# Kernel optimization log

Measured on AMD Instinct MI355X. Metric: run time of the kernel, lower is better.

Reference implementation:

```python
import jax, jax.numpy as jnp
import numpy as np

INF = 1e10  # sentinel 'infinity' for non-feature pixels (safe to add (s*N)^2 without overflow)


def _edt_sq_last(f, s):
    """Exact 1D squared distance transform along the last axis.
    f: (..., N) initialized to 0 at feature pixels, INF elsewhere.
    Returns g[..., i] = min_j f[..., j] + (s*(i-j))^2.
    Sequential lax.scan over output positions keeps memory at O(N) extra."""
    N = f.shape[-1]
    j = jnp.arange(N, dtype=f.dtype)

    def step(_, i):
        return None, jnp.min(f + (s * (i - j)) ** 2, axis=-1)

    _, out = jax.lax.scan(step, None, jnp.arange(N, dtype=f.dtype))
    return jnp.moveaxis(out, 0, -1)


def _edt(feature_mask, sampling):
    """Euclidean distance to the nearest True pixel of feature_mask (2D, anisotropic sampling).
    Equivalent to scipy.ndimage.distance_transform_edt(~feature_mask, sampling=sampling)."""
    f = jnp.where(feature_mask, 0.0, INF).astype(jnp.float32)
    # pass over axis -2 (rows), then axis -1 (cols) -- exact separable squared EDT
    f = jnp.moveaxis(_edt_sq_last(jnp.moveaxis(f, -2, -1), sampling[0]), -1, -2)
    f = _edt_sq_last(f, sampling[1])
    return jnp.sqrt(f)


def _distance_map(y_onehot, sampling):
    """res = edt_to_pos * negmask - (edt_to_neg - 1) * posmask, 0 where class absent."""
    pos = y_onehot              # (B,K,H,W) bool
    neg = ~pos
    d_neg = _edt(pos, sampling)  # distance of neg pixels to nearest pos pixel
    d_pos = _edt(neg, sampling)  # distance of pos pixels to nearest neg pixel
    res = jnp.where(neg, d_neg, 0.0) - jnp.where(pos, d_pos - 1.0, 0.0)
    has_pos = pos.any(axis=(-2, -1), keepdims=True)  # scipy path leaves res[k]=0 if class absent
    return jnp.where(has_pos, res, 0.0)


def reference(x, y):
    # x: (B,K,H,W) float; y: (B,1,H,W) int labels in [0,K)
    K = x.shape[1]
    y_onehot = (y == jnp.arange(K, dtype=y.dtype)[None, :, None, None])  # scatter_ onehot
    dist_map = jax.lax.stop_gradient(_distance_map(y_onehot, (1.0, 1.0)))
    return jnp.mean(x * dist_map)  # einsum('bkwh,bkwh->bkwh').mean()


def setup_inputs() -> dict:
    key = jax.random.key(0)
    k1, k2 = jax.random.split(key)
    x = jax.random.normal(k1, (8, 4, 256, 256), dtype=jnp.float32)
    y = jax.random.randint(k2, (8, 1, 256, 256), 0, 4, dtype=jnp.int32)
    return {"x": x, "y": y}
```

## Files before the change

### kernel.cpp

```cpp
#include <hip/hip_runtime.h>


#define HH 256
#define WW 256
#define NPIX (HH*WW)
#define NPM 64
#define BIG (1 << 27)

#define SEGS 16
#define RSEG 16
#define CPB 16

__global__ __launch_bounds__(256, 4) void edt_vpass(
        const int* __restrict__ y, unsigned short* __restrict__ g) {
    __shared__ unsigned short d[HH][CPB + 1];
    __shared__ short segLast[SEGS][CPB];
    __shared__ short segFirst[SEGS][CPB];

    int bid   = blockIdx.x;
    int pm    = bid >> 4;
    int cc    = bid & 15;
    int which = pm & 1;
    int plane = pm >> 1;
    int b     = plane >> 2;
    int k     = plane & 3;

    int t   = threadIdx.x;
    int col = t & (CPB - 1);
    int seg = t >> 4;
    int w   = cc * CPB + col;
    int h0  = seg * RSEG;

    const int* yp = y + b * NPIX;
    unsigned short* gp = g + (size_t)pm * NPIX;

    int lastL = -1000, firstL = 1000;
    for (int i = 0; i < RSEG; ++i) {
        int h   = h0 + i;
        int lab = yp[h * WW + w];
        int feat = ((lab == k) ? 1 : 0) ^ which;
        if (feat) { lastL = h; if (firstL > 900) firstL = h; }
        d[h][col] = (unsigned short)min(h - lastL, 1000);
    }
    segLast[seg][col]  = (short)lastL;
    segFirst[seg][col] = (short)firstL;
    __syncthreads();

    int prevLast = -1000;
    for (int s = seg - 1; s >= 0; --s) {
        int v = segLast[s][col];
        if (v >= 0) { prevLast = v; break; }
    }
    int nextFirst = 1000;
    for (int s = seg + 1; s < SEGS; ++s) {
        int v = segFirst[s][col];
        if (v < 900) { nextFirst = v; break; }
    }

    int nd = nextFirst;
    for (int i = RSEG - 1; i >= 0; --i) {
        int h  = h0 + i;
        int du = d[h][col];
        if (du == 0) nd = h;
        int dup = min(du, h - prevLast);
        int ddn = nd - h;
        int m   = min(min(dup, ddn), 256);
        gp[h * WW + w] = (m > 255) ? (unsigned short)0xFFFF
                                   : (unsigned short)(m * m);
    }
}

#define ROWS_PER_BLK 8
#define NBLK2 2048

__global__ void edt_hpass(const unsigned short* __restrict__ g,
                          const float* __restrict__ x,
                          double* __restrict__ bsums) {
    __shared__ int tile[ROWS_PER_BLK][WW];
    __shared__ double wsum[4];

    int bid   = blockIdx.x;
    int pm    = bid >> 5;
    int rc    = bid & 31;
    int r0    = rc * ROWS_PER_BLK;
    int which = pm & 1;
    int plane = pm >> 1;
    int t     = threadIdx.x;

    const unsigned short* gp = g + (size_t)pm * NPIX;
    const float* xp = x + (size_t)plane * NPIX;

    const unsigned int* gp32 = (const unsigned int*)(gp + r0 * WW);
    #pragma unroll
    for (int i2 = 0; i2 < 4; ++i2) {
        int idx = i2 * 256 + t;
        int row = idx >> 7;
        int c2  = idx & 127;
        unsigned int v = gp32[row * 128 + c2];
        int v0 = (int)(v & 0xFFFFu);
        int v1 = (int)(v >> 16);
        tile[row][2 * c2]     = (v0 == 0xFFFF) ? BIG : v0;
        tile[row][2 * c2 + 1] = (v1 == 0xFFFF) ? BIG : v1;
    }
    __syncthreads();

    double lsum = 0.0;
    for (int i = 0; i < ROWS_PER_BLK; ++i) {
        int best = tile[i][t];
        #pragma unroll 1
        for (int bs = 1; bs < WW; bs += 4) {
            if (bs * bs >= best) break;
            int m = best;
            #pragma unroll
            for (int u = 0; u < 4; ++u) {
                int r  = bs + u;
                int rr = r * r;
                int jl = max(t - r, 0);
                int jr = min(t + r, WW - 1);
                m = min(m, tile[i][jl] + rr);
                m = min(m, tile[i][jr] + rr);
            }
            best = m;
        }
        if (best > 0 && best < BIG) {
            float xv   = xp[(r0 + i) * WW + t];
            float dd   = sqrtf((float)best);
            float term = which ? (1.0f - dd) : dd;
            lsum += (double)(xv * term);
        }
    }

    for (int off = 32; off > 0; off >>= 1)
        lsum += __shfl_down(lsum, off, 64);
    int lane = t & 63, wv = t >> 6;
    if (lane == 0) wsum[wv] = lsum;
    __syncthreads();
    if (t == 0) bsums[bid] = wsum[0] + wsum[1] + wsum[2] + wsum[3];
}

__global__ void edt_finalize(const double* __restrict__ bsums, float* __restrict__ out) {
    __shared__ double wsum[4];
    int t = threadIdx.x;
    double s = 0.0;
    for (int i = t; i < NBLK2; i += 256) s += bsums[i];
    for (int off = 32; off > 0; off >>= 1)
        s += __shfl_down(s, off, 64);
    int lane = t & 63, wv = t >> 6;
    if (lane == 0) wsum[wv] = s;
    __syncthreads();
    if (t == 0)
        out[0] = (float)((wsum[0] + wsum[1] + wsum[2] + wsum[3]) * (1.0 / 2097152.0));
}

extern "C" void kernel_launch(void* const* d_in, const int* in_sizes, int n_in,
                              void* d_out, int out_size, void* d_ws, size_t ws_size,
                              hipStream_t stream) {
    const float* x = (const float*)d_in[0];
    const int*   y = (const int*)d_in[1];
    float* out = (float*)d_out;

    unsigned short* g = (unsigned short*)d_ws;
    double* bsums = (double*)((char*)d_ws + (size_t)NPM * NPIX * sizeof(unsigned short));

    edt_vpass   <<<1024,  256, 0, stream>>>(y, g);
    edt_hpass   <<<NBLK2, 256, 0, stream>>>(g, x, bsums);
    edt_finalize<<<1,     256, 0, stream>>>(bsums, out);
}
```

Baseline: 74.49 us.

## Process positive and negative masks together in one block per plane

Both the vertical and horizontal EDT passes now handle the feature mask and its complement in the same thread, packing the two 16-bit squared distances into one 32-bit word. This halves the number of blocks, reads the labels and x only once per plane, and merges the two contributions per pixel before accumulating. The cost is that each block does twice the serial work, with more registers and shared memory and fewer blocks to spread across the GPU. In the horizontal pass the two search loops run one after the other, so their trip counts add up per thread.

```diff
diff --git a/kernel.cpp b/kernel.cpp
--- a/kernel.cpp
+++ b/kernel.cpp
@@ -4,7 +4,7 @@
 #define HH 256
 #define WW 256
 #define NPIX (HH*WW)
-#define NPM 64
+#define NPL 32
 #define BIG (1 << 27)
 
 #define SEGS 16
@@ -12,18 +12,16 @@
 #define CPB 16
 
 __global__ __launch_bounds__(256, 4) void edt_vpass(
-        const int* __restrict__ y, unsigned short* __restrict__ g) {
-    __shared__ unsigned short d[HH][CPB + 1];
-    __shared__ short segLast[SEGS][CPB];
-    __shared__ short segFirst[SEGS][CPB];
+        const int* __restrict__ y, unsigned int* __restrict__ g) {
+    __shared__ unsigned int d[HH][CPB + 1];
+    __shared__ short segLast0[SEGS][CPB], segFirst0[SEGS][CPB];
+    __shared__ short segLast1[SEGS][CPB], segFirst1[SEGS][CPB];
 
-    int bid   = blockIdx.x;
-    int pm    = bid >> 4;
-    int cc    = bid & 15;
-    int which = pm & 1;
-    int plane = pm >> 1;
-    int b     = plane >> 2;
-    int k     = plane & 3;
+    int bid = blockIdx.x;
+    int pm  = bid >> 4;
+    int cc  = bid & 15;
+    int b   = pm >> 2;
+    int k   = pm & 3;
 
     int t   = threadIdx.x;
     int col = t & (CPB - 1);
@@ -32,100 +30,128 @@
     int h0  = seg * RSEG;
 
     const int* yp = y + b * NPIX;
-    unsigned short* gp = g + (size_t)pm * NPIX;
+    unsigned int* gp = g + (size_t)pm * NPIX;
 
-    int lastL = -1000, firstL = 1000;
+    int last0 = -1000, first0 = 1000, last1 = -1000, first1 = 1000;
     for (int i = 0; i < RSEG; ++i) {
         int h   = h0 + i;
         int lab = yp[h * WW + w];
-        int feat = ((lab == k) ? 1 : 0) ^ which;
-        if (feat) { lastL = h; if (firstL > 900) firstL = h; }
-        d[h][col] = (unsigned short)min(h - lastL, 1000);
+        if (lab == k) { last0 = h; if (first0 > 900) first0 = h; }
+        else          { last1 = h; if (first1 > 900) first1 = h; }
+        unsigned int du0 = (unsigned int)min(h - last0, 1000);
+        unsigned int du1 = (unsigned int)min(h - last1, 1000);
+        d[h][col] = du0 | (du1 << 16);
     }
-    segLast[seg][col]  = (short)lastL;
-    segFirst[seg][col] = (short)firstL;
+    segLast0[seg][col] = (short)last0;  segFirst0[seg][col] = (short)first0;
+    segLast1[seg][col] = (short)last1;  segFirst1[seg][col] = (short)first1;
     __syncthreads();
 
-    int prevLast = -1000;
+    int prevLast0 = -1000, prevLast1 = -1000;
     for (int s = seg - 1; s >= 0; --s) {
-        int v = segLast[s][col];
-        if (v >= 0) { prevLast = v; break; }
+        int v = segLast0[s][col];
+        if (v >= 0) { prevLast0 = v; break; }
     }
-    int nextFirst = 1000;
+    for (int s = seg - 1; s >= 0; --s) {
+        int v = segLast1[s][col];
+        if (v >= 0) { prevLast1 = v; break; }
+    }
+    int nextFirst0 = 1000, nextFirst1 = 1000;
     for (int s = seg + 1; s < SEGS; ++s) {
-        int v = segFirst[s][col];
-        if (v < 900) { nextFirst = v; break; }
+        int v = segFirst0[s][col];
+        if (v < 900) { nextFirst0 = v; break; }
+    }
+    for (int s = seg + 1; s < SEGS; ++s) {
+        int v = segFirst1[s][col];
+        if (v < 900) { nextFirst1 = v; break; }
     }
 
-    int nd = nextFirst;
+    int nd0 = nextFirst0, nd1 = nextFirst1;
     for (int i = RSEG - 1; i >= 0; --i) {
-        int h  = h0 + i;
-        int du = d[h][col];
-        if (du == 0) nd = h;
-        int dup = min(du, h - prevLast);
-        int ddn = nd - h;
-        int m   = min(min(dup, ddn), 256);
-        gp[h * WW + w] = (m > 255) ? (unsigned short)0xFFFF
-                                   : (unsigned short)(m * m);
+        int h = h0 + i;
+        unsigned int pk = d[h][col];
+        int du0 = (int)(pk & 0xFFFFu), du1 = (int)(pk >> 16);
+        if (du0 == 0) nd0 = h;
+        if (du1 == 0) nd1 = h;
+        int m0 = min(min(min(du0, h - prevLast0), nd0 - h), 256);
+        int m1 = min(min(min(du1, h - prevLast1), nd1 - h), 256);
+        unsigned int v0 = (m0 > 255) ? 0xFFFFu : (unsigned int)(m0 * m0);
+        unsigned int v1 = (m1 > 255) ? 0xFFFFu : (unsigned int)(m1 * m1);
+        gp[h * WW + w] = v0 | (v1 << 16);
     }
 }
 
 #define ROWS_PER_BLK 8
-#define NBLK2 2048
+#define NBLK2 1024
 
-__global__ void edt_hpass(const unsigned short* __restrict__ g,
+__global__ void edt_hpass(const unsigned int* __restrict__ g,
                           const float* __restrict__ x,
                           double* __restrict__ bsums) {
-    __shared__ int tile[ROWS_PER_BLK][WW];
+    __shared__ int t0[ROWS_PER_BLK][WW];
+    __shared__ int t1[ROWS_PER_BLK][WW];
     __shared__ double wsum[4];
 
-    int bid   = blockIdx.x;
-    int pm    = bid >> 5;
-    int rc    = bid & 31;
-    int r0    = rc * ROWS_PER_BLK;
-    int which = pm & 1;
-    int plane = pm >> 1;
-    int t     = threadIdx.x;
+    int bid = blockIdx.x;
+    int pm  = bid >> 5;
+    int rc  = bid & 31;
+    int r0  = rc * ROWS_PER_BLK;
+    int t   = threadIdx.x;
 
-    const unsigned short* gp = g + (size_t)pm * NPIX;
-    const float* xp = x + (size_t)plane * NPIX;
+    const unsigned int* gp = g + (size_t)pm * NPIX + r0 * WW;
+    const float* xp = x + (size_t)pm * NPIX;
 
-    const unsigned int* gp32 = (const unsigned int*)(gp + r0 * WW);
     #pragma unroll
-    for (int i2 = 0; i2 < 4; ++i2) {
+    for (int i2 = 0; i2 < 8; ++i2) {
         int idx = i2 * 256 + t;
-        int row = idx >> 7;
-        int c2  = idx & 127;
-        unsigned int v = gp32[row * 128 + c2];
+        int row = idx >> 8;
+        int c   = idx & 255;
+        unsigned int v = gp[row * WW + c];
         int v0 = (int)(v & 0xFFFFu);
         int v1 = (int)(v >> 16);
-        tile[row][2 * c2]     = (v0 == 0xFFFF) ? BIG : v0;
-        tile[row][2 * c2 + 1] = (v1 == 0xFFFF) ? BIG : v1;
+        t0[row][c] = (v0 == 0xFFFF) ? BIG : v0;
+        t1[row][c] = (v1 == 0xFFFF) ? BIG : v1;
     }
     __syncthreads();
 
     double lsum = 0.0;
     for (int i = 0; i < ROWS_PER_BLK; ++i) {
-        int best = tile[i][t];
+        int best0 = t0[i][t];
         #pragma unroll 1
         for (int bs = 1; bs < WW; bs += 4) {
-            if (bs * bs >= best) break;
-            int m = best;
+            if (bs * bs >= best0) break;
+            int m = best0;
             #pragma unroll
             for (int u = 0; u < 4; ++u) {
                 int r  = bs + u;
                 int rr = r * r;
                 int jl = max(t - r, 0);
                 int jr = min(t + r, WW - 1);
-                m = min(m, tile[i][jl] + rr);
-                m = min(m, tile[i][jr] + rr);
+                m = min(m, t0[i][jl] + rr);
+                m = min(m, t0[i][jr] + rr);
             }
-            best = m;
+            best0 = m;
         }
-        if (best > 0 && best < BIG) {
+        int best1 = t1[i][t];
+        #pragma unroll 1
+        for (int bs = 1; bs < WW; bs += 4) {
+            if (bs * bs >= best1) break;
+            int m = best1;
+            #pragma unroll
+            for (int u = 0; u < 4; ++u) {
+                int r  = bs + u;
+                int rr = r * r;
+                int jl = max(t - r, 0);
+                int jr = min(t + r, WW - 1);
+                m = min(m, t1[i][jl] + rr);
+                m = min(m, t1[i][jr] + rr);
+            }
+            best1 = m;
+        }
+        bool c0 = (best0 > 0) && (best0 < BIG);
+        bool c1 = (best1 > 0) && (best1 < BIG);
+        if (c0 | c1) {
             float xv   = xp[(r0 + i) * WW + t];
-            float dd   = sqrtf((float)best);
-            float term = which ? (1.0f - dd) : dd;
+            float term = c0 ? sqrtf((float)best0)
+                            : (1.0f - sqrtf((float)best1));
             lsum += (double)(xv * term);
         }
     }
@@ -159,10 +185,10 @@
     const int*   y = (const int*)d_in[1];
     float* out = (float*)d_out;
 
-    unsigned short* g = (unsigned short*)d_ws;
-    double* bsums = (double*)((char*)d_ws + (size_t)NPM * NPIX * sizeof(unsigned short));
+    unsigned int* g = (unsigned int*)d_ws;
+    double* bsums = (double*)((char*)d_ws + (size_t)NPL * NPIX * sizeof(unsigned int));
 
-    edt_vpass   <<<1024,  256, 0, stream>>>(y, g);
+    edt_vpass   <<<512,   256, 0, stream>>>(y, g);
     edt_hpass   <<<NBLK2, 256, 0, stream>>>(g, x, bsums);
     edt_finalize<<<1,     256, 0, stream>>>(bsums, out);
 }
```

Result: slower. 77.72 us (+4.3%).
